# Optimization experiments

Hardware: AMD Instinct MI355X
Metric: run time of the kernel (lower is better)

The kernel has to match this reference:

```python
import jax, jax.numpy as jnp
import numpy as np

NEG_SLOPE = 0.2  # PyG GATConv default
BN_EPS = 1e-5
NUM_GRAPHS = 128


def _bn(x, g, b, m, v):
    # eval-mode BatchNorm1d with running stats
    return (x - m) * jax.lax.rsqrt(v + BN_EPS) * g + b


def _gat_conv(x, src, dst, mask, W, a_src, a_dst, bias):
    # PyG GATConv: per-head linear, edge logits LeakyReLU(a_src.Wx_j + a_dst.Wx_i),
    # segment-softmax over incoming edges of each dst node, scatter-add messages.
    N = x.shape[0]
    H, C = a_src.shape
    xw = (x @ W).reshape(N, H, C)                       # [N,H,C]
    logit_s = (xw * a_src).sum(-1)                      # [N,H]
    logit_d = (xw * a_dst).sum(-1)                      # [N,H]
    e = jax.nn.leaky_relu(logit_s[src] + logit_d[dst], NEG_SLOPE)  # [E,H]
    e = jnp.where(mask[:, None], e, -1e30)              # edges filtered by edge_weights==1
    m = jax.ops.segment_max(e, dst, num_segments=N)     # [N,H]
    m = jnp.maximum(m, -1e30)                           # guard empty segments
    p = jnp.exp(e - m[dst]) * mask[:, None].astype(e.dtype)
    denom = jax.ops.segment_sum(p, dst, num_segments=N) + 1e-16
    alpha = p / denom[dst]                              # [E,H]
    out = jax.ops.segment_sum(xw[src] * alpha[..., None], dst, num_segments=N)
    return out.reshape(N, H * C) + bias


def setup_inputs() -> dict:
    key = jax.random.key(0)
    ks = jax.random.split(key, 20)
    N, E, F, G, NC = 20000, 320000, 128, NUM_GRAPHS, 10
    E0, E1, H = 256, 512, 2
    C = E1 // H

    def lin(k, fi, fo):
        return jax.random.normal(k, (fi, fo), jnp.float32) / np.float32(np.sqrt(fi))

    def bn(k, n):
        k1, k2, k3, k4 = jax.random.split(k, 4)
        g = 1.0 + 0.1 * jax.random.normal(k1, (n,), jnp.float32)
        b = 0.1 * jax.random.normal(k2, (n,), jnp.float32)
        m = 0.1 * jax.random.normal(k3, (n,), jnp.float32)
        v = 1.0 + 0.5 * jax.random.uniform(k4, (n,), jnp.float32)
        return g, b, m, v

    d = {}
    d['x'] = jax.random.normal(ks[0], (N, F), jnp.float32)
    d['edge_index'] = jax.random.randint(ks[1], (2, E), 0, N, dtype=jnp.int32)
    d['edge_weights'] = jnp.ones((E,), jnp.int32)
    d['batch'] = jnp.sort(jax.random.randint(ks[2], (N,), 0, G, dtype=jnp.int32))
    d['mlp_w1'] = lin(ks[3], F, E0); d['mlp_b1'] = jnp.zeros((E0,), jnp.float32)
    d['bn1_g'], d['bn1_b'], d['bn1_m'], d['bn1_v'] = bn(ks[4], E0)
    d['mlp_w2'] = lin(ks[5], E0, E0); d['mlp_b2'] = jnp.zeros((E0,), jnp.float32)
    d['bn2_g'], d['bn2_b'], d['bn2_m'], d['bn2_v'] = bn(ks[6], E0)
    d['gat0_w'] = lin(ks[7], E0, H * C)
    d['gat0_asrc'] = 0.1 * jax.random.normal(ks[8], (H, C), jnp.float32)
    d['gat0_adst'] = 0.1 * jax.random.normal(ks[9], (H, C), jnp.float32)
    d['gat0_bias'] = jnp.zeros((H * C,), jnp.float32)
    d['gat1_w'] = lin(ks[10], E1, H * C)
    d['gat1_asrc'] = 0.1 * jax.random.normal(ks[11], (H, C), jnp.float32)
    d['gat1_adst'] = 0.1 * jax.random.normal(ks[12], (H, C), jnp.float32)
    d['gat1_bias'] = jnp.zeros((H * C,), jnp.float32)
    d['bn3_g'], d['bn3_b'], d['bn3_m'], d['bn3_v'] = bn(ks[13], E1)
    d['fin_w1'] = lin(ks[14], E1, E1); d['fin_b1'] = jnp.zeros((E1,), jnp.float32)
    d['fin_w2'] = lin(ks[15], E1, NC); d['fin_b2'] = jnp.zeros((NC,), jnp.float32)
    return d


def reference(x, edge_index, edge_weights, batch,
              mlp_w1, mlp_b1, bn1_g, bn1_b, bn1_m, bn1_v,
              mlp_w2, mlp_b2, bn2_g, bn2_b, bn2_m, bn2_v,
              gat0_w, gat0_asrc, gat0_adst, gat0_bias,
              gat1_w, gat1_asrc, gat1_adst, gat1_bias,
              bn3_g, bn3_b, bn3_m, bn3_v,
              fin_w1, fin_b1, fin_w2, fin_b2):
    src, dst = edge_index[0], edge_index[1]
    mask = edge_weights == 1
    # initial MLP (dropout is identity in eval)
    h = jax.nn.relu(_bn(x @ mlp_w1 + mlp_b1, bn1_g, bn1_b, bn1_m, bn1_v))
    h = jax.nn.relu(_bn(h @ mlp_w2 + mlp_b2, bn2_g, bn2_b, bn2_m, bn2_v))
    # GAT layers
    h = _gat_conv(h, src, dst, mask, gat0_w, gat0_asrc, gat0_adst, gat0_bias)
    h = _gat_conv(h, src, dst, mask, gat1_w, gat1_asrc, gat1_adst, gat1_bias)
    # global mean pool over graphs
    sums = jax.ops.segment_sum(h, batch, num_segments=NUM_GRAPHS)
    cnt = jax.ops.segment_sum(jnp.ones((h.shape[0], 1), h.dtype), batch, num_segments=NUM_GRAPHS)
    pooled = sums / jnp.maximum(cnt, 1.0)
    # final head: BN -> ReLU -> Linear -> ReLU -> Linear
    z = jax.nn.relu(_bn(pooled, bn3_g, bn3_b, bn3_m, bn3_v))
    z = jax.nn.relu(z @ fin_w1 + fin_b1)
    return z @ fin_w2 + fin_b2
```

## Files before the change

kernel.cpp:

```cpp
#include <hip/hip_runtime.h>

typedef unsigned short u16;

constexpr int NN = 20000;
constexpr int EE = 320000;
constexpr int FD = 128;
constexpr int C0 = 256;
constexpr int C1 = 512;
constexpr int NG = 128;
constexpr int NC = 10;
constexpr int NBLK = (NN + 255) / 256;
constexpr int HB  = 320;
constexpr int EST = HB * 256;

constexpr size_t OFF_XB   = 0;
constexpr size_t OFF_H1   = OFF_XB  + (size_t)NN * FD * 2;
constexpr size_t OFF_H2   = OFF_H1  + (size_t)NN * C0 * 2;
constexpr size_t OFF_XW   = OFF_H2  + (size_t)NN * C0 * 2;
constexpr size_t OFF_H34  = OFF_XW  + (size_t)NN * C1 * 2;
constexpr size_t OFF_LS   = OFF_H34 + (size_t)NN * C1 * 2;
constexpr size_t OFF_LD   = OFF_LS  + (size_t)NN * 2 * 4;
constexpr size_t OFF_DEG  = OFF_LD  + (size_t)NN * 2 * 4;
constexpr size_t OFF_OFFS = OFF_DEG + (size_t)NN * 4;
constexpr size_t OFF_CUR  = OFF_OFFS + 80016;
constexpr size_t OFF_CSRC = OFF_CUR + (size_t)NN * 4;
constexpr size_t OFF_GCNT = OFF_CSRC + (size_t)EE * 4;
constexpr size_t OFF_GOFF = OFF_GCNT + 512;
constexpr size_t OFF_PART = OFF_GOFF + 768;
constexpr size_t OFF_PTOT = OFF_PART + 512;
constexpr size_t OFF_Z1   = OFF_PTOT + 256;
constexpr size_t OFF_Z2   = OFF_Z1  + (size_t)NG * C1 * 2;
constexpr size_t OFF_ST   = OFF_Z2  + (size_t)NG * C1 * 2;
constexpr size_t OFF_W1T  = OFF_ST  + 8192;
constexpr size_t OFF_W2T  = OFF_W1T + (size_t)FD * C0 * 2;
constexpr size_t OFF_G0T  = OFF_W2T + (size_t)C0 * C0 * 2;
constexpr size_t OFF_G1T  = OFF_G0T + (size_t)C0 * C1 * 2;
constexpr size_t OFF_AUX  = OFF_G1T + (size_t)C1 * C1 * 2;
constexpr size_t OFF_FLAG = OFF_AUX  + 0;
constexpr size_t OFF_A0S  = OFF_AUX  + 256;
constexpr size_t OFF_A0D  = OFF_AUX  + 1280;
constexpr size_t OFF_A1S  = OFF_AUX  + 2304;
constexpr size_t OFF_A1D  = OFF_AUX  + 3328;
constexpr size_t OFF_GB0  = OFF_AUX  + 4352;
constexpr size_t OFF_GB1  = OFF_AUX  + 6400;
constexpr size_t OFF_FB1  = OFF_AUX  + 8448;
constexpr size_t OFF_FB2  = OFF_AUX  + 10496;
constexpr size_t OFF_GMX  = OFF_AUX  + 10752;

__device__ inline float bf2f(u16 u) { return __uint_as_float(((unsigned)u) << 16); }
__device__ inline u16 f2bf(float f) {
    unsigned u = __float_as_uint(f);
    unsigned r = u + 0x7fffu + ((u >> 16) & 1u);
    return (u16)(r >> 16);
}
__device__ inline float ldf(const void* p, long i, unsigned f) {
    return f ? ((const float*)p)[i] : bf2f(((const u16*)p)[i]);
}
__device__ inline unsigned encf(float f) {
    unsigned u = __float_as_uint(f);
    return (u & 0x80000000u) ? ~u : (u | 0x80000000u);
}
__device__ inline float decf(unsigned e) {
    return (e & 0x80000000u) ? __uint_as_float(e ^ 0x80000000u) : __uint_as_float(~e);
}
__device__ inline void unpack8(uint4 r, float* v) {
    v[0] = bf2f((u16)(r.x & 0xffff)); v[1] = bf2f((u16)(r.x >> 16));
    v[2] = bf2f((u16)(r.y & 0xffff)); v[3] = bf2f((u16)(r.y >> 16));
    v[4] = bf2f((u16)(r.z & 0xffff)); v[5] = bf2f((u16)(r.z >> 16));
    v[6] = bf2f((u16)(r.w & 0xffff)); v[7] = bf2f((u16)(r.w >> 16));
}

typedef __bf16 bf16x8_t __attribute__((ext_vector_type(8)));
typedef float  f32x4_t  __attribute__((ext_vector_type(4)));

__device__ __forceinline__ void gl_lds16(const u16* g, u16* l) {
    __builtin_amdgcn_global_load_lds((const __attribute__((address_space(1))) void*)g,
                                     (__attribute__((address_space(3))) void*)l, 16, 0, 0);
}

__global__ void detect_dtype(const u16* __restrict__ x, const u16* __restrict__ w,
                             const u16* __restrict__ fw, unsigned* flag) {
    __shared__ int cnt;
    if (threadIdx.x == 0) cnt = 0;
    __syncthreads();
    int c = 0;
    for (int i = threadIdx.x; i < 4096; i += 256) {
        c += (((x[i]  >> 7) & 0xFF) == 0xFF);
        c += (((w[i]  >> 7) & 0xFF) == 0xFF);
        c += (((fw[i] >> 7) & 0xFF) == 0xFF);
    }
    atomicAdd(&cnt, c);
    __syncthreads();
    if (threadIdx.x == 0) *flag = (cnt >= 2) ? 1u : 0u;
}

__global__ void cvt_x(const unsigned* __restrict__ flag, const void* __restrict__ xin,
                      u16* __restrict__ XB, int* __restrict__ deg, int* __restrict__ gcnt,
                      unsigned* __restrict__ gmxu) {
    int i = blockIdx.x * 256 + threadIdx.x;
    if (i < NN) deg[i] = 0;
    if (i < NG) gcnt[i] = 0;
    if (i < 4)  gmxu[i] = encf(-1e30f);
    if (*flag) {
        float4 v = ((const float4*)xin)[i];
        ushort4 r;
        r.x = f2bf(v.x); r.y = f2bf(v.y); r.z = f2bf(v.z); r.w = f2bf(v.w);
        ((ushort4*)XB)[i] = r;
    } else {
        ((ushort4*)XB)[i] = ((const ushort4*)xin)[i];
    }
}

__global__ void prep_params(const unsigned* __restrict__ flag,
                            const void* g1, const void* b1, const void* m1, const void* v1, const void* lb1,
                            const void* g2, const void* b2, const void* m2, const void* v2, const void* lb2,
                            const void* g3, const void* b3, const void* m3, const void* v3,
                            const void* a0s, const void* a0d, const void* gb0in,
                            const void* a1s, const void* a1d, const void* gb1in,
                            const void* fb1in, const void* fb2in,
                            float* S1, float* T1, float* S2, float* T2, float* S3, float* T3,
                            u16* A0S, u16* A0D, u16* A1S, u16* A1D,
                            float* GB0, float* GB1, float* FB1, float* FB2) {
    unsigned f = *flag;
    int c = threadIdx.x;
    if (c < 256) {
        float s = ldf(g1, c, f) / sqrtf(ldf(v1, c, f) + 1e-5f);
        S1[c] = s; T1[c] = s * (ldf(lb1, c, f) - ldf(m1, c, f)) + ldf(b1, c, f);
        float s2 = ldf(g2, c, f) / sqrtf(ldf(v2, c, f) + 1e-5f);
        S2[c] = s2; T2[c] = s2 * (ldf(lb2, c, f) - ldf(m2, c, f)) + ldf(b2, c, f);
    }
    float s3 = ldf(g3, c, f) / sqrtf(ldf(v3, c, f) + 1e-5f);
    S3[c] = s3; T3[c] = ldf(b3, c, f) - ldf(m3, c, f) * s3;
    A0S[c] = f2bf(ldf(a0s, c, f));
    A0D[c] = f2bf(ldf(a0d, c, f));
    A1S[c] = f2bf(ldf(a1s, c, f));
    A1D[c] = f2bf(ldf(a1d, c, f));
    GB0[c] = ldf(gb0in, c, f);
    GB1[c] = ldf(gb1in, c, f);
    FB1[c] = ldf(fb1in, c, f);
    if (c < NC) FB2[c] = ldf(fb2in, c, f);
}

__global__ void transpose_all(const unsigned* __restrict__ flag,
                              const void* __restrict__ w1, const void* __restrict__ w2,
                              const void* __restrict__ g0, const void* __restrict__ g1,
                              u16* __restrict__ w1T, u16* __restrict__ w2T,
                              u16* __restrict__ g0T, u16* __restrict__ g1T) {
    int b = blockIdx.x;
    const void* B; u16* BT; int K, logN, base;
    if (b < 128)      { B = w1; BT = w1T; K = FD; logN = 8; base = 0; }
    else if (b < 384) { B = w2; BT = w2T; K = C0; logN = 8; base = 128; }
    else if (b < 896) { B = g0; BT = g0T; K = C0; logN = 9; base = 384; }
    else              { B = g1; BT = g1T; K = C1; logN = 9; base = 896; }
    int idx = (b - base) * 256 + threadIdx.x;
    int N = 1 << logN;
    int k = idx >> logN, n = idx & (N - 1);
    u16 v = (*flag) ? f2bf(((const float*)B)[idx]) : ((const u16*)B)[idx];
    BT[(size_t)n * K + k] = v;
}

__global__ __launch_bounds__(256) void hist_k(const int* __restrict__ dst, const int* __restrict__ ew,
                                              const int* __restrict__ batch,
                                              int* __restrict__ deg, int* __restrict__ gcnt) {
    int tid = blockIdx.x * 256 + threadIdx.x;
    int lane = threadIdx.x & 63;
#pragma unroll
    for (int j = 0; j < 4; j++) {
        int e = tid + j * EST;
        if (e < EE && ew[e] == 1) atomicAdd(&deg[dst[e]], 1);
    }
    int n = tid;
    if (n < NN) {
        int g = batch[n];
        int pg = __shfl_up(g, 1);
        bool head = (lane == 0) || (pg != g);
        unsigned long long act = __ballot(1);
        unsigned long long hm  = __ballot(head);
        if (head) {
            unsigned long long above = (lane < 63) ? ((hm >> (lane + 1)) << (lane + 1)) : 0ull;
            int limit = 64 - __builtin_clzll(act);
            int nxt = above ? __builtin_ctzll(above) : limit;
            atomicAdd(&gcnt[g], nxt - lane);
        }
    }
}
__global__ __launch_bounds__(256) void scan_blk(const int* __restrict__ deg, int* __restrict__ off,
                                                int* __restrict__ part) {
    __shared__ int tmp[256];
    int tid = threadIdx.x, i = blockIdx.x * 256 + tid;
    int v = (i < NN) ? deg[i] : 0;
    tmp[tid] = v;
    __syncthreads();
#pragma unroll
    for (int s = 1; s < 256; s <<= 1) {
        int a = (tid >= s) ? tmp[tid - s] : 0;
        __syncthreads();
        if (tid >= s) tmp[tid] += a;
        __syncthreads();
    }
    if (i < NN) off[i] = tmp[tid] - v;
    if (tid == 255) part[blockIdx.x] = tmp[255];
}
__global__ __launch_bounds__(128) void scan_small(int* __restrict__ part, int* __restrict__ ptot,
                                                  const int* __restrict__ gcnt, int* __restrict__ goff) {
    __shared__ int tmp[128];
    int tid = threadIdx.x;
    int v = (tid < NBLK) ? part[tid] : 0;
    tmp[tid] = v;
    __syncthreads();
#pragma unroll
    for (int s = 1; s < 128; s <<= 1) {
        int a = (tid >= s) ? tmp[tid - s] : 0;
        __syncthreads();
        if (tid >= s) tmp[tid] += a;
        __syncthreads();
    }
    if (tid < NBLK) part[tid] = tmp[tid] - v;
    if (tid == 127) *ptot = tmp[127];
    __syncthreads();
    int g = gcnt[tid];
    tmp[tid] = g;
    __syncthreads();
#pragma unroll
    for (int s = 1; s < 128; s <<= 1) {
        int a = (tid >= s) ? tmp[tid - s] : 0;
        __syncthreads();
        if (tid >= s) tmp[tid] += a;
        __syncthreads();
    }
    goff[tid] = tmp[tid] - g;
    if (tid == 127) goff[128] = tmp[127];
}
__global__ __launch_bounds__(256) void scan_add(int* __restrict__ off, const int* __restrict__ part,
                                                const int* __restrict__ ptot, int* __restrict__ cursor) {
    int tid = threadIdx.x, i = blockIdx.x * 256 + tid;
    if (i < NN) {
        int o = off[i] + part[blockIdx.x];
        off[i] = o;
        cursor[i] = o;
    }
    if (i == 0) off[NN] = *ptot;
}
__global__ __launch_bounds__(256) void csr_fill(const int* __restrict__ src, const int* __restrict__ dst,
                                                const int* __restrict__ ew,
                                                int* __restrict__ cursor, int* __restrict__ csrc) {
    int tid = blockIdx.x * 256 + threadIdx.x;
    bool ok[4]; int sv[4]; int p[4];
#pragma unroll
    for (int j = 0; j < 4; j++) {
        int e = tid + j * EST;
        ok[j] = false; sv[j] = 0; p[j] = 0;
        if (e < EE && ew[e] == 1) {
            ok[j] = true;
            sv[j] = src[e];
            p[j] = atomicAdd(&cursor[dst[e]], 1);
        }
    }
#pragma unroll
    for (int j = 0; j < 4; j++) if (ok[j]) csrc[p[j]] = sv[j];
}

template <int EPI>
__global__ __launch_bounds__(256) void gemm_tile(const u16* __restrict__ A, const u16* __restrict__ BT,
                                                 u16* __restrict__ Cm,
                                                 const float* __restrict__ S, const float* __restrict__ T,
                                                 int M, int N, int K) {
    __shared__ u16 As[128 * 32];
    __shared__ u16 Bs[128 * 32];
    const int tid  = threadIdx.x;
    const int wave = tid >> 6;
    const int lane = tid & 63;
    const int quad = lane >> 4;
    const int l16  = lane & 15;
    const int wr0  = (wave >> 1) * 64;
    const int wc0  = (wave & 1) * 64;
    const int row0 = blockIdx.x * 128;
    const int col0 = blockIdx.y * 128;

    const int lr = lane >> 2;
    const int lk = (lane & 3) * 8;
    int r0l = wave * 32 + lr;
    int r1l = r0l + 16;
    int gr0 = row0 + r0l; if (gr0 >= M) gr0 = M - 1;
    int gr1 = row0 + r1l; if (gr1 >= M) gr1 = M - 1;
    const u16* ga0 = A  + (size_t)gr0 * K + lk;
    const u16* ga1 = A  + (size_t)gr1 * K + lk;
    const u16* gb0 = BT + (size_t)(col0 + r0l) * K + lk;
    const u16* gb1 = BT + (size_t)(col0 + r1l) * K + lk;
    u16* la0 = As + (size_t)(wave * 32)      * 32 + lane * 8;
    u16* la1 = As + (size_t)(wave * 32 + 16) * 32 + lane * 8;
    u16* lb0 = Bs + (size_t)(wave * 32)      * 32 + lane * 8;
    u16* lb1 = Bs + (size_t)(wave * 32 + 16) * 32 + lane * 8;

    f32x4_t acc[4][4];
#pragma unroll
    for (int r = 0; r < 4; r++)
#pragma unroll
        for (int c = 0; c < 4; c++)
#pragma unroll
            for (int i = 0; i < 4; i++) acc[r][c][i] = 0.f;

    for (int k0 = 0; k0 < K; k0 += 32) {
        gl_lds16(ga0 + k0, la0);
        gl_lds16(ga1 + k0, la1);
        gl_lds16(gb0 + k0, lb0);
        gl_lds16(gb1 + k0, lb1);
        __syncthreads();

        bf16x8_t a[4], b[4];
#pragma unroll
        for (int r = 0; r < 4; r++)
            a[r] = *(const bf16x8_t*)(As + (size_t)(wr0 + r * 16 + l16) * 32 + quad * 8);
#pragma unroll
        for (int c = 0; c < 4; c++)
            b[c] = *(const bf16x8_t*)(Bs + (size_t)(wc0 + c * 16 + l16) * 32 + quad * 8);
#pragma unroll
        for (int r = 0; r < 4; r++)
#pragma unroll
            for (int c = 0; c < 4; c++)
                acc[r][c] = __builtin_amdgcn_mfma_f32_16x16x32_bf16(a[r], b[c], acc[r][c], 0, 0, 0);
        __syncthreads();
    }

#pragma unroll
    for (int r = 0; r < 4; r++) {
        int rb = row0 + wr0 + r * 16 + quad * 4;
#pragma unroll
        for (int c = 0; c < 4; c++) {
            int col = col0 + wc0 + c * 16 + l16;
            float sc = (EPI == 1) ? S[col] : 0.f;
            float sh = (EPI == 1) ? T[col] : 0.f;
#pragma unroll
            for (int i = 0; i < 4; i++) {
                int row = rb + i;
                if (row < M) {
                    float v = acc[r][c][i];
                    if (EPI == 1) v = fmaxf(v * sc + sh, 0.f);
                    Cm[(size_t)row * N + col] = f2bf(v);
                }
            }
        }
    }
}

__global__ __launch_bounds__(256) void gat_logits(const u16* __restrict__ xw, const u16* __restrict__ asrc,
                                                  const u16* __restrict__ adst, float* __restrict__ ls,
                                                  float* __restrict__ ld) {
    int n = blockIdx.x * 4 + (threadIdx.x >> 6);
    if (n >= NN) return;
    int lane = threadIdx.x & 63;
    uint4 xv = ((const uint4*)(xw + (size_t)n * C1))[lane];
    uint4 sv = ((const uint4*)asrc)[lane];
    uint4 dv = ((const uint4*)adst)[lane];
    float x[8], a[8], d[8];
    unpack8(xv, x); unpack8(sv, a); unpack8(dv, d);
    float ps = 0.f, pd = 0.f;
#pragma unroll
    for (int j = 0; j < 8; j++) { ps += x[j] * a[j]; pd += x[j] * d[j]; }
#pragma unroll
    for (int m = 16; m >= 1; m >>= 1) { ps += __shfl_xor(ps, m); pd += __shfl_xor(pd, m); }
    if ((lane & 31) == 0) {
        int h = lane >> 5;
        ls[n * 2 + h] = ps;
        ld[n * 2 + h] = pd;
    }
}

__global__ __launch_bounds__(256) void ls_max(const float* __restrict__ ls, unsigned* __restrict__ gmx) {
    int tid = blockIdx.x * 256 + threadIdx.x;
    float m0 = -1e30f, m1 = -1e30f;
    for (int n = tid; n < NN; n += 40 * 256) {
        float2 v = ((const float2*)ls)[n];
        m0 = fmaxf(m0, v.x); m1 = fmaxf(m1, v.y);
    }
#pragma unroll
    for (int o = 32; o >= 1; o >>= 1) {
        m0 = fmaxf(m0, __shfl_xor(m0, o));
        m1 = fmaxf(m1, __shfl_xor(m1, o));
    }
    if ((threadIdx.x & 63) == 0) {
        atomicMax(&gmx[0], encf(m0));
        atomicMax(&gmx[1], encf(m1));
    }
}

__device__ __forceinline__ void proc_edge(uint4 c, float lv, float ldh, float mhat,
                                          float* acc, float& den) {
    float v = lv + ldh;
    v = v > 0.f ? v : 0.2f * v;
    float p = __expf(v - mhat);
    den += p;
    float x[8];
    unpack8(c, x);
#pragma unroll
    for (int q = 0; q < 8; q++) acc[q] = fmaf(p, x[q], acc[q]);
}

__global__ __launch_bounds__(256) void gat_aggregate(const int* __restrict__ off, const int* __restrict__ csrc,
                                                     const float* __restrict__ ls, const float* __restrict__ ld,
                                                     const unsigned* __restrict__ gmx, const u16* __restrict__ xw,
                                                     const float* __restrict__ bias, u16* __restrict__ outh) {
    int n = blockIdx.x * 4 + (threadIdx.x >> 6);
    if (n >= NN) return;
    int lane = threadIdx.x & 63;
    int h = lane >> 5;
    int beg = off[n], end = off[n + 1];
    float ldh = ld[n * 2 + h];
    float gm = decf(gmx[h]) + ldh;
    float mhat = gm > 0.f ? gm : 0.2f * gm;

    float acc[8];
#pragma unroll
    for (int j = 0; j < 8; j++) acc[j] = 0.f;
    float den = 0.f;

#define ROWLD(S) (((const uint4*)(xw + (size_t)(S) * C1))[lane])

    for (int base = beg; base < end; base += 64) {
        int cnt = end - base; if (cnt > 64) cnt = 64;
        int e = base + lane;
        int ec = e < end ? e : end - 1;
        int sv = csrc[ec];
        float2 lp = ((const float2*)ls)[sv];

        uint4 r0 = ROWLD(__shfl(sv, 0));
        uint4 r1 = ROWLD(__shfl(sv, 1));
        uint4 r2 = ROWLD(__shfl(sv, 2));
        uint4 r3 = ROWLD(__shfl(sv, 3));

        for (int j = 0; j < cnt; j += 4) {
            uint4 c0 = r0, c1 = r1, c2 = r2, c3 = r3;
            float wx0 = __shfl(lp.x, j),            wy0 = __shfl(lp.y, j);
            float wx1 = __shfl(lp.x, (j + 1) & 63), wy1 = __shfl(lp.y, (j + 1) & 63);
            float wx2 = __shfl(lp.x, (j + 2) & 63), wy2 = __shfl(lp.y, (j + 2) & 63);
            float wx3 = __shfl(lp.x, (j + 3) & 63), wy3 = __shfl(lp.y, (j + 3) & 63);
            float w0 = h ? wy0 : wx0;
            float w1 = h ? wy1 : wx1;
            float w2 = h ? wy2 : wx2;
            float w3 = h ? wy3 : wx3;
            if (j + 4 < cnt) {
                r0 = ROWLD(__shfl(sv, (j + 4) & 63));
                r1 = ROWLD(__shfl(sv, (j + 5) & 63));
                r2 = ROWLD(__shfl(sv, (j + 6) & 63));
                r3 = ROWLD(__shfl(sv, (j + 7) & 63));
            }
            proc_edge(c0, w0, ldh, mhat, acc, den);
            if (j + 1 < cnt) proc_edge(c1, w1, ldh, mhat, acc, den);
            if (j + 2 < cnt) proc_edge(c2, w2, ldh, mhat, acc, den);
            if (j + 3 < cnt) proc_edge(c3, w3, ldh, mhat, acc, den);
        }
    }
#undef ROWLD

    float inv = 1.f / fmaxf(den, 1e-30f);
    ushort4 r0, r1;
    int cb = lane * 8;
    float o0 = acc[0] * inv + bias[cb + 0], o1 = acc[1] * inv + bias[cb + 1];
    float o2 = acc[2] * inv + bias[cb + 2], o3 = acc[3] * inv + bias[cb + 3];
    float o4 = acc[4] * inv + bias[cb + 4], o5 = acc[5] * inv + bias[cb + 5];
    float o6 = acc[6] * inv + bias[cb + 6], o7 = acc[7] * inv + bias[cb + 7];
    r0.x = f2bf(o0); r0.y = f2bf(o1); r0.z = f2bf(o2); r0.w = f2bf(o3);
    r1.x = f2bf(o4); r1.y = f2bf(o5); r1.z = f2bf(o6); r1.w = f2bf(o7);
    ushort4* dst4 = (ushort4*)(outh + (size_t)n * C1 + cb);
    dst4[0] = r0; dst4[1] = r1;
}

__global__ __launch_bounds__(512) void pool_bn(const u16* __restrict__ h4, const int* __restrict__ goff,
                                               const float* __restrict__ S3, const float* __restrict__ T3,
                                               u16* __restrict__ z1) {
    int g = blockIdx.x, t = threadIdx.x;
    int b = goff[g], e = goff[g + 1];
    float s = 0.f;
    for (int n = b; n < e; n++) s += bf2f(h4[(size_t)n * C1 + t]);
    float mean = s / fmaxf((float)(e - b), 1.f);
    float v = mean * S3[t] + T3[t];
    z1[(size_t)g * C1 + t] = f2bf(fmaxf(v, 0.f));
}

__global__ __launch_bounds__(512) void head_fc1(const unsigned* __restrict__ flag, const u16* __restrict__ z1,
                                                const void* __restrict__ w1, const float* __restrict__ FB1,
                                                u16* __restrict__ z2) {
    __shared__ float zrow[512];
    int g = blockIdx.x, t = threadIdx.x;
    zrow[t] = bf2f(z1[(size_t)g * 512 + t]);
    __syncthreads();
    float acc = 0.f;
    if (*flag) {
        const float* w = (const float*)w1;
        for (int k = 0; k < 512; k++) acc = fmaf(zrow[k], w[(size_t)k * 512 + t], acc);
    } else {
        const u16* w = (const u16*)w1;
        for (int k = 0; k < 512; k++) acc = fmaf(zrow[k], bf2f(w[(size_t)k * 512 + t]), acc);
    }
    acc += FB1[t];
    z2[(size_t)g * 512 + t] = f2bf(fmaxf(acc, 0.f));
}
__global__ __launch_bounds__(64) void head_fc2(const unsigned* __restrict__ flag, const u16* __restrict__ z2,
                                               const void* __restrict__ w2, const float* __restrict__ FB2,
                                               void* __restrict__ out) {
    int g = blockIdx.x, o = blockIdx.y, lane = threadIdx.x;
    unsigned f = *flag;
    float acc = 0.f;
    if (f) {
        const float* w = (const float*)w2;
        for (int k = lane; k < 512; k += 64) acc += bf2f(z2[(size_t)g * 512 + k]) * w[(size_t)k * NC + o];
    } else {
        const u16* w = (const u16*)w2;
        for (int k = lane; k < 512; k += 64) acc += bf2f(z2[(size_t)g * 512 + k]) * bf2f(w[(size_t)k * NC + o]);
    }
#pragma unroll
    for (int m = 32; m >= 1; m >>= 1) acc += __shfl_xor(acc, m);
    if (lane == 0) {
        float v = acc + FB2[o];
        if (f) ((float*)out)[g * NC + o] = v;
        else   ((u16*)out)[g * NC + o] = f2bf(v);
    }
}

extern "C" void kernel_launch(void* const* d_in, const int* in_sizes, int n_in,
                              void* d_out, int out_size, void* d_ws, size_t ws_size,
                              hipStream_t stream) {
    (void)in_sizes; (void)n_in; (void)out_size; (void)ws_size;

    const void* x      = d_in[0];
    const int* ei      = (const int*)d_in[1];
    const int* src     = ei;
    const int* dst     = ei + EE;
    const int* ew      = (const int*)d_in[2];
    const int* batch   = (const int*)d_in[3];
    const void* mlp_w1 = d_in[4];
    const void* mlp_b1 = d_in[5];
    const void *bn1g = d_in[6], *bn1b = d_in[7], *bn1m = d_in[8], *bn1v = d_in[9];
    const void* mlp_w2 = d_in[10];
    const void* mlp_b2 = d_in[11];
    const void *bn2g = d_in[12], *bn2b = d_in[13], *bn2m = d_in[14], *bn2v = d_in[15];
    const void* g0w    = d_in[16];
    const void* g0as   = d_in[17];
    const void* g0ad   = d_in[18];
    const void* g0bias = d_in[19];
    const void* g1w    = d_in[20];
    const void* g1as   = d_in[21];
    const void* g1ad   = d_in[22];
    const void* g1bias = d_in[23];
    const void *bn3g = d_in[24], *bn3b = d_in[25], *bn3m = d_in[26], *bn3v = d_in[27];
    const void* fin_w1 = d_in[28];
    const void* fin_b1 = d_in[29];
    const void* fin_w2 = d_in[30];
    const void* fin_b2 = d_in[31];

    char* ws = (char*)d_ws;
    u16*  XB   = (u16*)(ws + OFF_XB);
    u16*  h1   = (u16*)(ws + OFF_H1);
    u16*  h2   = (u16*)(ws + OFF_H2);
    u16*  xw   = (u16*)(ws + OFF_XW);
    u16*  h34  = (u16*)(ws + OFF_H34);
    float* ls  = (float*)(ws + OFF_LS);
    float* ld  = (float*)(ws + OFF_LD);
    int*  deg  = (int*)(ws + OFF_DEG);
    int*  off  = (int*)(ws + OFF_OFFS);
    int*  cur  = (int*)(ws + OFF_CUR);
    int*  csrc = (int*)(ws + OFF_CSRC);
    int*  gcnt = (int*)(ws + OFF_GCNT);
    int*  goff = (int*)(ws + OFF_GOFF);
    int*  part = (int*)(ws + OFF_PART);
    int*  ptot = (int*)(ws + OFF_PTOT);
    u16*  z1   = (u16*)(ws + OFF_Z1);
    u16*  z2   = (u16*)(ws + OFF_Z2);
    float* S1 = (float*)(ws + OFF_ST);
    float* T1 = S1 + 256;
    float* S2 = T1 + 256;
    float* T2 = S2 + 256;
    float* S3 = T2 + 256;
    float* T3 = S3 + 512;
    u16* w1T = (u16*)(ws + OFF_W1T);
    u16* w2T = (u16*)(ws + OFF_W2T);
    u16* g0T = (u16*)(ws + OFF_G0T);
    u16* g1T = (u16*)(ws + OFF_G1T);
    unsigned* flag = (unsigned*)(ws + OFF_FLAG);
    u16* A0S = (u16*)(ws + OFF_A0S);
    u16* A0D = (u16*)(ws + OFF_A0D);
    u16* A1S = (u16*)(ws + OFF_A1S);
    u16* A1D = (u16*)(ws + OFF_A1D);
    float* GB0 = (float*)(ws + OFF_GB0);
    float* GB1 = (float*)(ws + OFF_GB1);
    float* FB1 = (float*)(ws + OFF_FB1);
    float* FB2 = (float*)(ws + OFF_FB2);
    unsigned* GMXU = (unsigned*)(ws + OFF_GMX);

    detect_dtype<<<1, 256, 0, stream>>>((const u16*)x, (const u16*)mlp_w1, (const u16*)fin_w1, flag);
    cvt_x<<<(NN * FD / 4) / 256, 256, 0, stream>>>(flag, x, XB, deg, gcnt, GMXU);
    prep_params<<<1, 512, 0, stream>>>(flag,
                                       bn1g, bn1b, bn1m, bn1v, mlp_b1,
                                       bn2g, bn2b, bn2m, bn2v, mlp_b2,
                                       bn3g, bn3b, bn3m, bn3v,
                                       g0as, g0ad, g0bias, g1as, g1ad, g1bias,
                                       fin_b1, fin_b2,
                                       S1, T1, S2, T2, S3, T3,
                                       A0S, A0D, A1S, A1D, GB0, GB1, FB1, FB2);
    transpose_all<<<1920, 256, 0, stream>>>(flag, mlp_w1, mlp_w2, g0w, g1w, w1T, w2T, g0T, g1T);

    hist_k<<<HB, 256, 0, stream>>>(dst, ew, batch, deg, gcnt);
    scan_blk<<<NBLK, 256, 0, stream>>>(deg, off, part);
    scan_small<<<1, 128, 0, stream>>>(part, ptot, gcnt, goff);
    scan_add<<<NBLK, 256, 0, stream>>>(off, part, ptot, cur);
    csr_fill<<<HB, 256, 0, stream>>>(src, dst, ew, cur, csrc);

    gemm_tile<1><<<dim3(157, 2), 256, 0, stream>>>(XB, w1T, h1, S1, T1, NN, C0, FD);
    gemm_tile<1><<<dim3(157, 2), 256, 0, stream>>>(h1, w2T, h2, S2, T2, NN, C0, C0);

    gemm_tile<0><<<dim3(157, 4), 256, 0, stream>>>(h2, g0T, xw, nullptr, nullptr, NN, C1, C0);
    gat_logits<<<NN / 4, 256, 0, stream>>>(xw, A0S, A0D, ls, ld);
    ls_max<<<40, 256, 0, stream>>>(ls, GMXU);
    gat_aggregate<<<NN / 4, 256, 0, stream>>>(off, csrc, ls, ld, GMXU, xw, GB0, h34);

    gemm_tile<0><<<dim3(157, 4), 256, 0, stream>>>(h34, g1T, xw, nullptr, nullptr, NN, C1, C1);
    gat_logits<<<NN / 4, 256, 0, stream>>>(xw, A1S, A1D, ls, ld);
    ls_max<<<40, 256, 0, stream>>>(ls, GMXU + 2);
    gat_aggregate<<<NN / 4, 256, 0, stream>>>(off, csrc, ls, ld, GMXU + 2, xw, GB1, h34);

    pool_bn<<<NG, 512, 0, stream>>>(h34, goff, S3, T3, z1);
    head_fc1<<<NG, 512, 0, stream>>>(flag, z1, fin_w1, FB1, z2);
    head_fc2<<<dim3(NG, NC), 64, 0, stream>>>(flag, z2, fin_w2, FB2, d_out);
}
```

Measured before the change: 416.2 us.

## Fuse logit max into gat_logits and compute edge weights per-lane in aggregate

```diff
diff --git a/kernel.cpp b/kernel.cpp
--- a/kernel.cpp
+++ b/kernel.cpp
@@ -12,6 +12,8 @@
 constexpr int NBLK = (NN + 255) / 256;
 constexpr int HB  = 320;
 constexpr int EST = HB * 256;
+constexpr int AGB = 2048;
+constexpr int LGB = 640;
 
 constexpr size_t OFF_XB   = 0;
 constexpr size_t OFF_H1   = OFF_XB  + (size_t)NN * FD * 2;
@@ -64,10 +66,10 @@
     return (e & 0x80000000u) ? __uint_as_float(e ^ 0x80000000u) : __uint_as_float(~e);
 }
 __device__ inline void unpack8(uint4 r, float* v) {
-    v[0] = bf2f((u16)(r.x & 0xffff)); v[1] = bf2f((u16)(r.x >> 16));
-    v[2] = bf2f((u16)(r.y & 0xffff)); v[3] = bf2f((u16)(r.y >> 16));
-    v[4] = bf2f((u16)(r.z & 0xffff)); v[5] = bf2f((u16)(r.z >> 16));
-    v[6] = bf2f((u16)(r.w & 0xffff)); v[7] = bf2f((u16)(r.w >> 16));
+    v[0] = __uint_as_float(r.x << 16); v[1] = __uint_as_float(r.x & 0xffff0000u);
+    v[2] = __uint_as_float(r.y << 16); v[3] = __uint_as_float(r.y & 0xffff0000u);
+    v[4] = __uint_as_float(r.z << 16); v[5] = __uint_as_float(r.z & 0xffff0000u);
+    v[6] = __uint_as_float(r.w << 16); v[7] = __uint_as_float(r.w & 0xffff0000u);
 }
 
 typedef __bf16 bf16x8_t __attribute__((ext_vector_type(8)));
@@ -345,124 +347,123 @@
 
 __global__ __launch_bounds__(256) void gat_logits(const u16* __restrict__ xw, const u16* __restrict__ asrc,
                                                   const u16* __restrict__ adst, float* __restrict__ ls,
-                                                  float* __restrict__ ld) {
-    int n = blockIdx.x * 4 + (threadIdx.x >> 6);
-    if (n >= NN) return;
+                                                  float* __restrict__ ld, unsigned* __restrict__ gmx) {
+    __shared__ float smax[8];
     int lane = threadIdx.x & 63;
-    uint4 xv = ((const uint4*)(xw + (size_t)n * C1))[lane];
-    uint4 sv = ((const uint4*)asrc)[lane];
+    int wv   = threadIdx.x >> 6;
+    int h    = lane >> 5;
+    uint4 av = ((const uint4*)asrc)[lane];
     uint4 dv = ((const uint4*)adst)[lane];
-    float x[8], a[8], d[8];
-    unpack8(xv, x); unpack8(sv, a); unpack8(dv, d);
-    float ps = 0.f, pd = 0.f;
-#pragma unroll
-    for (int j = 0; j < 8; j++) { ps += x[j] * a[j]; pd += x[j] * d[j]; }
-#pragma unroll
-    for (int m = 16; m >= 1; m >>= 1) { ps += __shfl_xor(ps, m); pd += __shfl_xor(pd, m); }
-    if ((lane & 31) == 0) {
-        int h = lane >> 5;
-        ls[n * 2 + h] = ps;
-        ld[n * 2 + h] = pd;
-    }
-}
-
-__global__ __launch_bounds__(256) void ls_max(const float* __restrict__ ls, unsigned* __restrict__ gmx) {
-    int tid = blockIdx.x * 256 + threadIdx.x;
-    float m0 = -1e30f, m1 = -1e30f;
-    for (int n = tid; n < NN; n += 40 * 256) {
-        float2 v = ((const float2*)ls)[n];
-        m0 = fmaxf(m0, v.x); m1 = fmaxf(m1, v.y);
-    }
-#pragma unroll
-    for (int o = 32; o >= 1; o >>= 1) {
-        m0 = fmaxf(m0, __shfl_xor(m0, o));
-        m1 = fmaxf(m1, __shfl_xor(m1, o));
-    }
-    if ((threadIdx.x & 63) == 0) {
-        atomicMax(&gmx[0], encf(m0));
-        atomicMax(&gmx[1], encf(m1));
-    }
-}
-
-__device__ __forceinline__ void proc_edge(uint4 c, float lv, float ldh, float mhat,
-                                          float* acc, float& den) {
-    float v = lv + ldh;
-    v = v > 0.f ? v : 0.2f * v;
-    float p = __expf(v - mhat);
-    den += p;
+    float a[8], d[8];
+    unpack8(av, a); unpack8(dv, d);
+    float mm = -1e30f;
+    int n = blockIdx.x * 4 + wv;
+    uint4 xv;
+    if (n < NN) xv = ((const uint4*)(xw + (size_t)n * C1))[lane];
+    while (n < NN) {
+        int n2 = n + LGB * 4;
+        uint4 nx;
+        if (n2 < NN) nx = ((const uint4*)(xw + (size_t)n2 * C1))[lane];
+        float x[8];
+        unpack8(xv, x);
+        float ps = 0.f, pd = 0.f;
+#pragma unroll
+        for (int j = 0; j < 8; j++) { ps += x[j] * a[j]; pd += x[j] * d[j]; }
+#pragma unroll
+        for (int m = 16; m >= 1; m >>= 1) { ps += __shfl_xor(ps, m); pd += __shfl_xor(pd, m); }
+        if ((lane & 31) == 0) {
+            ls[n * 2 + h] = ps;
+            ld[n * 2 + h] = pd;
+        }
+        mm = fmaxf(mm, ps);
+        xv = nx; n = n2;
+    }
+    if ((lane & 31) == 0) smax[wv * 2 + h] = mm;
+    __syncthreads();
+    if (threadIdx.x < 2) {
+        float m = fmaxf(fmaxf(smax[threadIdx.x], smax[2 + threadIdx.x]),
+                        fmaxf(smax[4 + threadIdx.x], smax[6 + threadIdx.x]));
+        atomicMax(&gmx[threadIdx.x], encf(m));
+    }
+}
+
+__device__ __forceinline__ void proc_edge(uint4 c, float w, float* acc, float& den) {
+    den += w;
     float x[8];
     unpack8(c, x);
 #pragma unroll
-    for (int q = 0; q < 8; q++) acc[q] = fmaf(p, x[q], acc[q]);
-}
-
-__global__ __launch_bounds__(256) void gat_aggregate(const int* __restrict__ off, const int* __restrict__ csrc,
-                                                     const float* __restrict__ ls, const float* __restrict__ ld,
-                                                     const unsigned* __restrict__ gmx, const u16* __restrict__ xw,
-                                                     const float* __restrict__ bias, u16* __restrict__ outh) {
-    int n = blockIdx.x * 4 + (threadIdx.x >> 6);
-    if (n >= NN) return;
-    int lane = threadIdx.x & 63;
-    int h = lane >> 5;
-    int beg = off[n], end = off[n + 1];
-    float ldh = ld[n * 2 + h];
-    float gm = decf(gmx[h]) + ldh;
-    float mhat = gm > 0.f ? gm : 0.2f * gm;
-
-    float acc[8];
-#pragma unroll
-    for (int j = 0; j < 8; j++) acc[j] = 0.f;
-    float den = 0.f;
+    for (int q = 0; q < 8; q++) acc[q] = fmaf(w, x[q], acc[q]);
+}
+
+__global__ __launch_bounds__(256, 8) void gat_aggregate(const int* __restrict__ off, const int* __restrict__ csrc,
+                                                        const float* __restrict__ ls, const float* __restrict__ ld,
+                                                        const unsigned* __restrict__ gmx, const u16* __restrict__ xw,
+                                                        const float* __restrict__ bias, u16* __restrict__ outh) {
+    const int lane = threadIdx.x & 63;
+    const int h    = lane >> 5;
+    const int el   = lane & 31;
+    const int hoff = h << 5;
+    const float gmax = decf(gmx[h]);
+    const int cb = lane * 8;
 
 #define ROWLD(S) (((const uint4*)(xw + (size_t)(S) * C1))[lane])
 
-    for (int base = beg; base < end; base += 64) {
-        int cnt = end - base; if (cnt > 64) cnt = 64;
-        int e = base + lane;
-        int ec = e < end ? e : end - 1;
-        int sv = csrc[ec];
-        float2 lp = ((const float2*)ls)[sv];
-
-        uint4 r0 = ROWLD(__shfl(sv, 0));
-        uint4 r1 = ROWLD(__shfl(sv, 1));
-        uint4 r2 = ROWLD(__shfl(sv, 2));
-        uint4 r3 = ROWLD(__shfl(sv, 3));
-
-        for (int j = 0; j < cnt; j += 4) {
-            uint4 c0 = r0, c1 = r1, c2 = r2, c3 = r3;
-            float wx0 = __shfl(lp.x, j),            wy0 = __shfl(lp.y, j);
-            float wx1 = __shfl(lp.x, (j + 1) & 63), wy1 = __shfl(lp.y, (j + 1) & 63);
-            float wx2 = __shfl(lp.x, (j + 2) & 63), wy2 = __shfl(lp.y, (j + 2) & 63);
-            float wx3 = __shfl(lp.x, (j + 3) & 63), wy3 = __shfl(lp.y, (j + 3) & 63);
-            float w0 = h ? wy0 : wx0;
-            float w1 = h ? wy1 : wx1;
-            float w2 = h ? wy2 : wx2;
-            float w3 = h ? wy3 : wx3;
-            if (j + 4 < cnt) {
-                r0 = ROWLD(__shfl(sv, (j + 4) & 63));
-                r1 = ROWLD(__shfl(sv, (j + 5) & 63));
-                r2 = ROWLD(__shfl(sv, (j + 6) & 63));
-                r3 = ROWLD(__shfl(sv, (j + 7) & 63));
+    for (int n = blockIdx.x * 4 + (threadIdx.x >> 6); n < NN; n += AGB * 4) {
+        int beg = off[n], end = off[n + 1];
+        float2 ldv = ((const float2*)ld)[n];
+        float ldh = h ? ldv.y : ldv.x;
+        float gm = gmax + ldh;
+        float mhat = gm > 0.f ? gm : 0.2f * gm;
+
+        float acc[8];
+#pragma unroll
+        for (int q = 0; q < 8; q++) acc[q] = 0.f;
+        float den = 0.f;
+
+        for (int base = beg; base < end; base += 32) {
+            int cnt = end - base; if (cnt > 32) cnt = 32;
+            int e = base + el;
+            int ec = e < end ? e : end - 1;
+            int sv = csrc[ec];
+            float vv = ls[sv * 2 + h] + ldh;
+            vv = vv > 0.f ? vv : 0.2f * vv;
+            float myp = __expf(vv - mhat);
+
+            uint4 r0 = ROWLD(__shfl(sv, 0));
+            uint4 r1 = ROWLD(__shfl(sv, 1));
+            uint4 r2 = ROWLD(__shfl(sv, 2));
+            uint4 r3 = ROWLD(__shfl(sv, 3));
+
+            for (int j = 0; j < cnt; j += 4) {
+                uint4 c0 = r0, c1 = r1, c2 = r2, c3 = r3;
+                float w0 = __shfl(myp, j + hoff);
+                float w1 = __shfl(myp, j + 1 + hoff);
+                float w2 = __shfl(myp, j + 2 + hoff);
+                float w3 = __shfl(myp, j + 3 + hoff);
+                if (j + 4 < cnt) {
+                    r0 = ROWLD(__shfl(sv, j + 4));
+                    r1 = ROWLD(__shfl(sv, j + 5));
+                    r2 = ROWLD(__shfl(sv, j + 6));
+                    r3 = ROWLD(__shfl(sv, j + 7));
+                }
+                proc_edge(c0, w0, acc, den);
+                if (j + 1 < cnt) proc_edge(c1, w1, acc, den);
+                if (j + 2 < cnt) proc_edge(c2, w2, acc, den);
+                if (j + 3 < cnt) proc_edge(c3, w3, acc, den);
             }
-            proc_edge(c0, w0, ldh, mhat, acc, den);
-            if (j + 1 < cnt) proc_edge(c1, w1, ldh, mhat, acc, den);
-            if (j + 2 < cnt) proc_edge(c2, w2, ldh, mhat, acc, den);
-            if (j + 3 < cnt) proc_edge(c3, w3, ldh, mhat, acc, den);
         }
+
+        float inv = 1.f / fmaxf(den, 1e-30f);
+        const float4* bp = (const float4*)(bias + cb);
+        float4 b0 = bp[0], b1 = bp[1];
+        uint4 st;
+        st.x = (unsigned)f2bf(acc[0] * inv + b0.x) | ((unsigned)f2bf(acc[1] * inv + b0.y) << 16);
+        st.y = (unsigned)f2bf(acc[2] * inv + b0.z) | ((unsigned)f2bf(acc[3] * inv + b0.w) << 16);
+        st.z = (unsigned)f2bf(acc[4] * inv + b1.x) | ((unsigned)f2bf(acc[5] * inv + b1.y) << 16);
+        st.w = (unsigned)f2bf(acc[6] * inv + b1.z) | ((unsigned)f2bf(acc[7] * inv + b1.w) << 16);
+        ((uint4*)(outh + (size_t)n * C1 + cb))[0] = st;
     }
 #undef ROWLD
-
-    float inv = 1.f / fmaxf(den, 1e-30f);
-    ushort4 r0, r1;
-    int cb = lane * 8;
-    float o0 = acc[0] * inv + bias[cb + 0], o1 = acc[1] * inv + bias[cb + 1];
-    float o2 = acc[2] * inv + bias[cb + 2], o3 = acc[3] * inv + bias[cb + 3];
-    float o4 = acc[4] * inv + bias[cb + 4], o5 = acc[5] * inv + bias[cb + 5];
-    float o6 = acc[6] * inv + bias[cb + 6], o7 = acc[7] * inv + bias[cb + 7];
-    r0.x = f2bf(o0); r0.y = f2bf(o1); r0.z = f2bf(o2); r0.w = f2bf(o3);
-    r1.x = f2bf(o4); r1.y = f2bf(o5); r1.z = f2bf(o6); r1.w = f2bf(o7);
-    ushort4* dst4 = (ushort4*)(outh + (size_t)n * C1 + cb);
-    dst4[0] = r0; dst4[1] = r1;
 }
 
 __global__ __launch_bounds__(512) void pool_bn(const u16* __restrict__ h4, const int* __restrict__ goff,
@@ -609,14 +610,12 @@
     gemm_tile<1><<<dim3(157, 2), 256, 0, stream>>>(h1, w2T, h2, S2, T2, NN, C0, C0);
 
     gemm_tile<0><<<dim3(157, 4), 256, 0, stream>>>(h2, g0T, xw, nullptr, nullptr, NN, C1, C0);
-    gat_logits<<<NN / 4, 256, 0, stream>>>(xw, A0S, A0D, ls, ld);
-    ls_max<<<40, 256, 0, stream>>>(ls, GMXU);
-    gat_aggregate<<<NN / 4, 256, 0, stream>>>(off, csrc, ls, ld, GMXU, xw, GB0, h34);
+    gat_logits<<<LGB, 256, 0, stream>>>(xw, A0S, A0D, ls, ld, GMXU);
+    gat_aggregate<<<AGB, 256, 0, stream>>>(off, csrc, ls, ld, GMXU, xw, GB0, h34);
 
     gemm_tile<0><<<dim3(157, 4), 256, 0, stream>>>(h34, g1T, xw, nullptr, nullptr, NN, C1, C1);
-    gat_logits<<<NN / 4, 256, 0, stream>>>(xw, A1S, A1D, ls, ld);
-    ls_max<<<40, 256, 0, stream>>>(ls, GMXU + 2);
-    gat_aggregate<<<NN / 4, 256, 0, stream>>>(off, csrc, ls, ld, GMXU + 2, xw, GB1, h34);
+    gat_logits<<<LGB, 256, 0, stream>>>(xw, A1S, A1D, ls, ld, GMXU + 2);
+    gat_aggregate<<<AGB, 256, 0, stream>>>(off, csrc, ls, ld, GMXU + 2, xw, GB1, h34);
 
     pool_bn<<<NG, 512, 0, stream>>>(h34, goff, S3, T3, z1);
     head_fc1<<<NG, 512, 0, stream>>>(flag, z1, fin_w1, FB1, z2);
```

New measurement: 474.2 us. 13.9% more time.
